# Performance work log

Hardware: AMD Instinct MI355X
Metric: run time of the kernel (lower is better)

Reference implementation:

```python
import jax, jax.numpy as jnp
import numpy as np

N, M, D = 65536, 2048, 256

def setup_inputs() -> dict:
    key = jax.random.key(0)
    k1, k2 = jax.random.split(key)
    memory = jax.random.normal(k1, (M, D), dtype=jnp.float32)
    query = jax.random.normal(k2, (N, D), dtype=jnp.float32)
    return {"memory": memory, "query": query}

def reference(memory, query):
    # score: [N, M] = query @ memory^T
    score = jnp.matmul(query.astype(jnp.float32), memory.astype(jnp.float32).T)
    # softmax over memory slots (dim=1); scores are detached in the original
    softmax_score_memory = jax.nn.softmax(score, axis=1)
    # read from memory: [N, M] @ [M, D] -> [N, D]
    concat_memory = jnp.matmul(softmax_score_memory, memory)
    return concat_memory
```

## Files before the change

kernel.cpp:

```cpp
#include <hip/hip_runtime.h>

typedef _Float16 f16;
typedef __attribute__((ext_vector_type(8))) _Float16 f16x8;
typedef __attribute__((ext_vector_type(16))) float f32x16;
typedef __attribute__((ext_vector_type(4))) unsigned u32x4;

#define MM 2048
#define DD 256
#define LOG2E 1.44269504088896340736f

__device__ __forceinline__ void gload_lds16(const void* g, void* l) {
    __builtin_amdgcn_global_load_lds(
        (const __attribute__((address_space(1))) unsigned int*)g,
        (__attribute__((address_space(3))) unsigned int*)l, 16, 0, 0);
}
__device__ __forceinline__ f32x16 mfma32(f16x8 a, f16x8 b, f32x16 c) {
    return __builtin_amdgcn_mfma_f32_32x32x16_f16(a, b, c, 0, 0, 0);
}
__device__ __forceinline__ void plswap(unsigned& a, unsigned& b) {
    asm volatile("v_permlane32_swap_b32 %0, %1" : "+v"(a), "+v"(b));
}
__device__ __forceinline__ unsigned pk2(float a, float b) {
    return __builtin_bit_cast(unsigned, __builtin_amdgcn_cvt_pkrtz(a, b));
}

__global__ void prep_kernel(const float* __restrict__ mem,
                            f16* __restrict__ kprep, f16* __restrict__ vtprep) {
    int t = blockIdx.x * blockDim.x + threadIdx.x;
    if (t < 65536) {
        int b = t >> 10, r = t & 1023, u = r >> 5, kk = r & 31;
        const float* src = mem + (b * 32 + kk) * DD + u * 8;
        f16 o8[8];
#pragma unroll
        for (int e = 0; e < 8; ++e) o8[e] = (f16)src[e];
        *(f16x8*)(kprep + (size_t)t * 8) = *(f16x8*)o8;
    } else {
        int t2 = t - 65536;
        int b = t2 >> 10, r = t2 & 1023, u = r >> 8, d = r & 255;
        f16 o8[8];
#pragma unroll
        for (int e = 0; e < 8; ++e) o8[e] = (f16)mem[(b * 32 + u * 8 + e) * DD + d];
        *(f16x8*)(vtprep + (size_t)t2 * 8) = *(f16x8*)o8;
    }
}

__launch_bounds__(512, 2)
__global__ void attn_kernel(const float* __restrict__ q,
                            const f16* __restrict__ kprep,
                            const f16* __restrict__ vtprep,
                            float* __restrict__ out) {
    __shared__ __align__(16) f16 klds[4][8192];
    __shared__ __align__(16) f16 vtlds[4][8192];

    const int tid = threadIdx.x;
    const int w = __builtin_amdgcn_readfirstlane(tid >> 6);
    const int lane = tid & 63;
    const int h = lane >> 5;
    const int l31 = lane & 31;
    const int q0 = blockIdx.x * 256 + w * 32;

    f16x8 qf[16];
#pragma unroll
    for (int s = 0; s < 16; ++s) {
        const float* src = q + (size_t)(q0 + l31) * DD + s * 16 + h * 8;
        float4 a = *(const float4*)src;
        float4 b2 = *(const float4*)(src + 4);
        f16 t8[8] = {(f16)a.x, (f16)a.y, (f16)a.z, (f16)a.w,
                     (f16)b2.x, (f16)b2.y, (f16)b2.z, (f16)b2.w};
        qf[s] = *(f16x8*)t8;
    }

    f32x16 o[8];
#pragma unroll
    for (int dt = 0; dt < 8; ++dt) o[dt] = (f32x16)(0.f);
    float lpart = 0.f, mrun = -1e30f;
    f16x8 pa0 = (f16x8)(f16)0.f, pa1 = (f16x8)(f16)0.f;

#define STAGE_K(t_)                                                       \
    do {                                                                  \
        const f16* s_ = kprep + (size_t)(t_)*8192;                        \
        _Pragma("unroll")                                                 \
        for (int i_ = 0; i_ < 2; ++i_)                                    \
            gload_lds16(s_ + i_ * 4096 + w * 512 + lane * 8,              \
                        &klds[(t_) & 3][i_ * 4096 + w * 512]);            \
    } while (0)
#define STAGE_VT(t_)                                                      \
    do {                                                                  \
        const f16* s_ = vtprep + (size_t)(t_)*8192;                       \
        _Pragma("unroll")                                                 \
        for (int i_ = 0; i_ < 2; ++i_)                                    \
            gload_lds16(s_ + i_ * 4096 + w * 512 + lane * 8,              \
                        &vtlds[(t_) & 3][i_ * 4096 + w * 512]);           \
    } while (0)

#define QK(t_, s_)                                                            \
    do {                                                                      \
        const f16* kb_ = &klds[(t_) & 3][0];                                  \
        _Pragma("unroll")                                                     \
        for (int st_ = 0; st_ < 16; ++st_) {                                  \
            f16x8 ak_ = *(const f16x8*)(kb_ + ((2 * st_ + h) * 32 + l31) * 8);\
            s_ = mfma32(ak_, qf[st_], s_);                                    \
        }                                                                     \
    } while (0)

#define PV(t_)                                                                 \
    do {                                                                       \
        const f16* vb_ = &vtlds[(t_) & 3][0];                                  \
        _Pragma("unroll")                                                      \
        for (int dt_ = 0; dt_ < 8; ++dt_) {                                    \
            f16x8 v0_ = *(const f16x8*)(vb_ + ((0 + h) * 256 + dt_ * 32 + l31) * 8); \
            f16x8 v1_ = *(const f16x8*)(vb_ + ((2 + h) * 256 + dt_ * 32 + l31) * 8); \
            o[dt_] = mfma32(pa0, v0_, o[dt_]);                                 \
            o[dt_] = mfma32(pa1, v1_, o[dt_]);                                 \
        }                                                                      \
    } while (0)

#define SOFTMAX_PACK(s_)                                                       \
    do {                                                                       \
        float sm_ = s_[0];                                                     \
        _Pragma("unroll") for (int r_ = 1; r_ < 16; ++r_)                      \
            sm_ = fmaxf(sm_, s_[r_]);                                          \
        sm_ *= LOG2E;                                                          \
        if (__any(sm_ > mrun + 8.0f)) {                                        \
            sm_ = fmaxf(sm_, __shfl_xor(sm_, 32));                             \
            const float mn_ = fmaxf(mrun, sm_);                                \
            const float fct_ = __builtin_amdgcn_exp2f(mrun - mn_);             \
            mrun = mn_;                                                        \
            lpart *= fct_;                                                     \
            float fr_[16];                                                     \
            _Pragma("unroll") for (int r_ = 0; r_ < 16; ++r_)                  \
                fr_[r_] = __shfl(fct_, (r_ & 3) + 8 * (r_ >> 2) + 4 * h, 32);  \
            _Pragma("unroll") for (int dt_ = 0; dt_ < 8; ++dt_)                \
                _Pragma("unroll") for (int r_ = 0; r_ < 16; ++r_)              \
                    o[dt_][r_] *= fr_[r_];                                     \
        }                                                                      \
        float p_[16], rs_ = 0.f;                                               \
        _Pragma("unroll") for (int r_ = 0; r_ < 16; ++r_) {                    \
            p_[r_] = __builtin_amdgcn_exp2f(                                   \
                __builtin_fmaf(s_[r_], LOG2E, -mrun));                         \
            rs_ += p_[r_];                                                     \
        }                                                                      \
        lpart += rs_;                                                          \
        unsigned c0_ = pk2(p_[0], p_[1]), c1_ = pk2(p_[2], p_[3]);             \
        unsigned c2_ = pk2(p_[4], p_[5]), c3_ = pk2(p_[6], p_[7]);             \
        unsigned c4_ = pk2(p_[8], p_[9]), c5_ = pk2(p_[10], p_[11]);           \
        unsigned c6_ = pk2(p_[12], p_[13]), c7_ = pk2(p_[14], p_[15]);         \
        plswap(c0_, c2_); plswap(c1_, c3_);                                    \
        plswap(c4_, c6_); plswap(c5_, c7_);                                    \
        u32x4 k0_ = {c0_, c1_, c2_, c3_}, k1_ = {c4_, c5_, c6_, c7_};          \
        pa0 = __builtin_bit_cast(f16x8, k0_);                                  \
        pa1 = __builtin_bit_cast(f16x8, k1_);                                  \
    } while (0)

    STAGE_K(0);
    STAGE_K(1);
    STAGE_VT(0);

    for (int p = 0; p < 32; ++p) {
        const int t0 = 2 * p, t1 = 2 * p + 1;
        __syncthreads();
        if (p < 31) { STAGE_K(t0 + 2); STAGE_K(t1 + 2); }
        STAGE_VT(t1);
        if (p < 31) STAGE_VT(t1 + 1);

        __builtin_amdgcn_s_setprio(1);
        f32x16 s0 = (f32x16)(0.f);
        QK(t0, s0);
        if (p) PV(t0 - 1);
        __builtin_amdgcn_s_setprio(0);
        SOFTMAX_PACK(s0);

        __builtin_amdgcn_s_setprio(1);
        f32x16 s1 = (f32x16)(0.f);
        QK(t1, s1);
        PV(t0);
        __builtin_amdgcn_s_setprio(0);
        SOFTMAX_PACK(s1);
    }

    __syncthreads();
    __builtin_amdgcn_s_setprio(1);
    PV(63);
    __builtin_amdgcn_s_setprio(0);

    const float ltot = lpart + __shfl_xor(lpart, 32);
    const float inv = 1.0f / ltot;
    float invr[16];
#pragma unroll
    for (int r = 0; r < 16; ++r)
        invr[r] = __shfl(inv, (r & 3) + 8 * (r >> 2) + 4 * h, 32);
#pragma unroll
    for (int dt = 0; dt < 8; ++dt)
#pragma unroll
        for (int r = 0; r < 16; ++r) {
            const int qrow = (r & 3) + 8 * (r >> 2) + 4 * h;
            out[(size_t)(q0 + qrow) * DD + dt * 32 + l31] = o[dt][r] * invr[r];
        }
}

extern "C" void kernel_launch(void* const* d_in, const int* in_sizes, int n_in,
                              void* d_out, int out_size, void* d_ws, size_t ws_size,
                              hipStream_t stream) {
    const float* memory = (const float*)d_in[0];
    const float* query = (const float*)d_in[1];
    float* out = (float*)d_out;
    f16* kprep = (f16*)d_ws;
    f16* vtprep = kprep + (size_t)MM * DD;
    prep_kernel<<<512, 256, 0, stream>>>(memory, kprep, vtprep);
    attn_kernel<<<256, 512, 0, stream>>>(query, kprep, vtprep, out);
}
```

Before: 150.9 us.

## Restructure main loop into fine-grained barrier-phased QK/PV pipeline with explicit waits

Replaces the two-tile-per-iteration loop with a per-tile schedule split into four barrier-separated phases: two halves of QK and two halves of PV. Each phase issues its LDS reads and global-to-LDS prefetch before the MFMAs, using sched_barrier, s_barrier and explicit vmcnt waits. The V^T LDS buffer shrinks from four to two stages. The aim is to interleave memory traffic and MFMA work across waves in lockstep and to cut LDS use. The cost is many more block-wide barriers per tile and a fragile dependence on hand-counted vmcnt values, where a wrong count causes LDS races.

```diff
diff --git a/kernel.cpp b/kernel.cpp
--- a/kernel.cpp
+++ b/kernel.cpp
@@ -23,6 +23,8 @@
 __device__ __forceinline__ unsigned pk2(float a, float b) {
     return __builtin_bit_cast(unsigned, __builtin_amdgcn_cvt_pkrtz(a, b));
 }
+#define SB() __builtin_amdgcn_sched_barrier(0)
+#define BAR() __builtin_amdgcn_s_barrier()
 
 __global__ void prep_kernel(const float* __restrict__ mem,
                             f16* __restrict__ kprep, f16* __restrict__ vtprep) {
@@ -50,7 +52,7 @@
                             const f16* __restrict__ vtprep,
                             float* __restrict__ out) {
     __shared__ __align__(16) f16 klds[4][8192];
-    __shared__ __align__(16) f16 vtlds[4][8192];
+    __shared__ __align__(16) f16 vtlds[2][8192];
 
     const int tid = threadIdx.x;
     const int w = __builtin_amdgcn_readfirstlane(tid >> 6);
@@ -78,7 +80,7 @@
 
 #define STAGE_K(t_)                                                       \
     do {                                                                  \
-        const f16* s_ = kprep + (size_t)(t_)*8192;                        \
+        const f16* s_ = kprep + (size_t)((t_)&63) * 8192;                 \
         _Pragma("unroll")                                                 \
         for (int i_ = 0; i_ < 2; ++i_)                                    \
             gload_lds16(s_ + i_ * 4096 + w * 512 + lane * 8,              \
@@ -90,30 +92,12 @@
         _Pragma("unroll")                                                 \
         for (int i_ = 0; i_ < 2; ++i_)                                    \
             gload_lds16(s_ + i_ * 4096 + w * 512 + lane * 8,              \
-                        &vtlds[(t_) & 3][i_ * 4096 + w * 512]);           \
+                        &vtlds[(t_) & 1][i_ * 4096 + w * 512]);           \
     } while (0)
 
-#define QK(t_, s_)                                                            \
-    do {                                                                      \
-        const f16* kb_ = &klds[(t_) & 3][0];                                  \
-        _Pragma("unroll")                                                     \
-        for (int st_ = 0; st_ < 16; ++st_) {                                  \
-            f16x8 ak_ = *(const f16x8*)(kb_ + ((2 * st_ + h) * 32 + l31) * 8);\
-            s_ = mfma32(ak_, qf[st_], s_);                                    \
-        }                                                                     \
-    } while (0)
-
-#define PV(t_)                                                                 \
-    do {                                                                       \
-        const f16* vb_ = &vtlds[(t_) & 3][0];                                  \
-        _Pragma("unroll")                                                      \
-        for (int dt_ = 0; dt_ < 8; ++dt_) {                                    \
-            f16x8 v0_ = *(const f16x8*)(vb_ + ((0 + h) * 256 + dt_ * 32 + l31) * 8); \
-            f16x8 v1_ = *(const f16x8*)(vb_ + ((2 + h) * 256 + dt_ * 32 + l31) * 8); \
-            o[dt_] = mfma32(pa0, v0_, o[dt_]);                                 \
-            o[dt_] = mfma32(pa1, v1_, o[dt_]);                                 \
-        }                                                                      \
-    } while (0)
+#define RD_K(t_, st_) (*(const f16x8*)(&klds[(t_)&3][((2 * (st_) + h) * 32 + l31) * 8]))
+#define RD_V0(t_, d_) (*(const f16x8*)(&vtlds[(t_)&1][((0 + h) * 256 + (d_)*32 + l31) * 8]))
+#define RD_V1(t_, d_) (*(const f16x8*)(&vtlds[(t_)&1][((2 + h) * 256 + (d_)*32 + l31) * 8]))
 
 #define SOFTMAX_PACK(s_)                                                       \
     do {                                                                       \
@@ -154,33 +138,111 @@
 
     STAGE_K(0);
     STAGE_K(1);
-    STAGE_VT(0);
-
-    for (int p = 0; p < 32; ++p) {
-        const int t0 = 2 * p, t1 = 2 * p + 1;
-        __syncthreads();
-        if (p < 31) { STAGE_K(t0 + 2); STAGE_K(t1 + 2); }
-        STAGE_VT(t1);
-        if (p < 31) STAGE_VT(t1 + 1);
-
-        __builtin_amdgcn_s_setprio(1);
-        f32x16 s0 = (f32x16)(0.f);
-        QK(t0, s0);
-        if (p) PV(t0 - 1);
-        __builtin_amdgcn_s_setprio(0);
-        SOFTMAX_PACK(s0);
-
-        __builtin_amdgcn_s_setprio(1);
-        f32x16 s1 = (f32x16)(0.f);
-        QK(t1, s1);
-        PV(t0);
-        __builtin_amdgcn_s_setprio(0);
-        SOFTMAX_PACK(s1);
-    }
-
-    __syncthreads();
+
+    {
+        asm volatile("s_waitcnt vmcnt(2)" ::: "memory");
+        SB(); BAR(); SB();
+        f32x16 s = (f32x16)(0.f);
+        {
+            f16x8 a0 = RD_K(0, 0), a1 = RD_K(0, 1), a2 = RD_K(0, 2), a3 = RD_K(0, 3);
+            f16x8 a4 = RD_K(0, 4), a5 = RD_K(0, 5), a6 = RD_K(0, 6), a7 = RD_K(0, 7);
+            STAGE_K(2);
+            SB(); BAR(); SB();
+            __builtin_amdgcn_s_setprio(1);
+            s = mfma32(a0, qf[0], s); s = mfma32(a1, qf[1], s);
+            s = mfma32(a2, qf[2], s); s = mfma32(a3, qf[3], s);
+            s = mfma32(a4, qf[4], s); s = mfma32(a5, qf[5], s);
+            s = mfma32(a6, qf[6], s); s = mfma32(a7, qf[7], s);
+            __builtin_amdgcn_s_setprio(0);
+            BAR();
+        }
+        {
+            f16x8 a0 = RD_K(0, 8), a1 = RD_K(0, 9), a2 = RD_K(0, 10), a3 = RD_K(0, 11);
+            f16x8 a4 = RD_K(0, 12), a5 = RD_K(0, 13), a6 = RD_K(0, 14), a7 = RD_K(0, 15);
+            STAGE_VT(0);
+            SB(); BAR(); SB();
+            __builtin_amdgcn_s_setprio(1);
+            s = mfma32(a0, qf[8], s); s = mfma32(a1, qf[9], s);
+            s = mfma32(a2, qf[10], s); s = mfma32(a3, qf[11], s);
+            s = mfma32(a4, qf[12], s); s = mfma32(a5, qf[13], s);
+            s = mfma32(a6, qf[14], s); s = mfma32(a7, qf[15], s);
+            __builtin_amdgcn_s_setprio(0);
+            BAR();
+        }
+        SOFTMAX_PACK(s);
+        asm volatile("s_waitcnt vmcnt(4)" ::: "memory");
+        SB(); BAR(); SB();
+    }
+
+    for (int t = 1; t < 64; ++t) {
+        f32x16 s = (f32x16)(0.f);
+        {
+            f16x8 a0 = RD_K(t, 0), a1 = RD_K(t, 1), a2 = RD_K(t, 2), a3 = RD_K(t, 3);
+            f16x8 a4 = RD_K(t, 4), a5 = RD_K(t, 5), a6 = RD_K(t, 6), a7 = RD_K(t, 7);
+            STAGE_K(t + 2);
+            SB(); BAR(); SB();
+            __builtin_amdgcn_s_setprio(1);
+            s = mfma32(a0, qf[0], s); s = mfma32(a1, qf[1], s);
+            s = mfma32(a2, qf[2], s); s = mfma32(a3, qf[3], s);
+            s = mfma32(a4, qf[4], s); s = mfma32(a5, qf[5], s);
+            s = mfma32(a6, qf[6], s); s = mfma32(a7, qf[7], s);
+            __builtin_amdgcn_s_setprio(0);
+            BAR();
+        }
+        {
+            f16x8 a0 = RD_K(t, 8), a1 = RD_K(t, 9), a2 = RD_K(t, 10), a3 = RD_K(t, 11);
+            f16x8 a4 = RD_K(t, 12), a5 = RD_K(t, 13), a6 = RD_K(t, 14), a7 = RD_K(t, 15);
+            STAGE_VT(t);
+            SB(); BAR(); SB();
+            __builtin_amdgcn_s_setprio(1);
+            s = mfma32(a0, qf[8], s); s = mfma32(a1, qf[9], s);
+            s = mfma32(a2, qf[10], s); s = mfma32(a3, qf[11], s);
+            s = mfma32(a4, qf[12], s); s = mfma32(a5, qf[13], s);
+            s = mfma32(a6, qf[14], s); s = mfma32(a7, qf[15], s);
+            __builtin_amdgcn_s_setprio(0);
+            BAR();
+        }
+        {
+            asm volatile("s_waitcnt vmcnt(4)" ::: "memory");
+            SB(); BAR(); SB();
+            f16x8 v00 = RD_V0(t - 1, 0), v10 = RD_V1(t - 1, 0);
+            f16x8 v01 = RD_V0(t - 1, 1), v11 = RD_V1(t - 1, 1);
+            f16x8 v02 = RD_V0(t - 1, 2), v12 = RD_V1(t - 1, 2);
+            f16x8 v03 = RD_V0(t - 1, 3), v13 = RD_V1(t - 1, 3);
+            __builtin_amdgcn_s_setprio(1);
+            o[0] = mfma32(pa0, v00, o[0]); o[0] = mfma32(pa1, v10, o[0]);
+            o[1] = mfma32(pa0, v01, o[1]); o[1] = mfma32(pa1, v11, o[1]);
+            o[2] = mfma32(pa0, v02, o[2]); o[2] = mfma32(pa1, v12, o[2]);
+            o[3] = mfma32(pa0, v03, o[3]); o[3] = mfma32(pa1, v13, o[3]);
+            __builtin_amdgcn_s_setprio(0);
+            BAR();
+        }
+        {
+            f16x8 v04 = RD_V0(t - 1, 4), v14 = RD_V1(t - 1, 4);
+            f16x8 v05 = RD_V0(t - 1, 5), v15 = RD_V1(t - 1, 5);
+            f16x8 v06 = RD_V0(t - 1, 6), v16 = RD_V1(t - 1, 6);
+            f16x8 v07 = RD_V0(t - 1, 7), v17 = RD_V1(t - 1, 7);
+            SB(); BAR(); SB();
+            __builtin_amdgcn_s_setprio(1);
+            o[4] = mfma32(pa0, v04, o[4]); o[4] = mfma32(pa1, v14, o[4]);
+            o[5] = mfma32(pa0, v05, o[5]); o[5] = mfma32(pa1, v15, o[5]);
+            o[6] = mfma32(pa0, v06, o[6]); o[6] = mfma32(pa1, v16, o[6]);
+            o[7] = mfma32(pa0, v07, o[7]); o[7] = mfma32(pa1, v17, o[7]);
+            __builtin_amdgcn_s_setprio(0);
+            BAR();
+        }
+        SOFTMAX_PACK(s);
+    }
+
+    asm volatile("s_waitcnt vmcnt(0)" ::: "memory");
+    SB(); BAR(); SB();
     __builtin_amdgcn_s_setprio(1);
-    PV(63);
+#pragma unroll
+    for (int dt = 0; dt < 8; ++dt) {
+        f16x8 v0 = RD_V0(63, dt), v1 = RD_V1(63, dt);
+        o[dt] = mfma32(pa0, v0, o[dt]);
+        o[dt] = mfma32(pa1, v1, o[dt]);
+    }
     __builtin_amdgcn_s_setprio(0);
 
     const float ltot = lpart + __shfl_xor(lpart, 32);
```

Result: slower. 194.5 us (+28.9%).
